# Performance work log

Hardware: AMD Instinct MI355X
Metric: run time of the kernel (lower is better)

The kernel has to match this reference:

```python
import jax, jax.numpy as jnp
import numpy as np

DIM = 512
N_GROUPS = 8
N_CODES = 1024
SUB = DIM // N_GROUPS
CB_LAMBDA = 1.0
COMMIT_LAMBDA = 0.25


def setup_inputs() -> dict:
    key = jax.random.key(0)
    k1, k2, k3 = jax.random.split(key, 3)
    x = jax.random.normal(k1, (8, DIM, 4096), dtype=jnp.float32)
    lim = 1.0 / N_CODES
    codebooks1 = jax.random.uniform(k2, (N_GROUPS, N_CODES, SUB), dtype=jnp.float32, minval=-lim, maxval=lim)
    codebooks2 = jax.random.uniform(k3, (N_GROUPS, N_CODES, SUB), dtype=jnp.float32, minval=-lim, maxval=lim)
    return {"x": x, "codebooks1": codebooks1, "codebooks2": codebooks2}


def _quantize_group(flat, cbs):
    # flat: (N, G, d), cbs: (G, K, d)
    x2 = jnp.sum(flat * flat, axis=-1, keepdims=True)          # (N, G, 1)
    e2 = jnp.sum(cbs * cbs, axis=-1)                            # (G, K)
    xe = jnp.einsum('ngd,gkd->ngk', flat, cbs)                  # (N, G, K)
    d = x2 + e2[None, :, :] - 2.0 * xe                          # (N, G, K)
    idx = jnp.argmin(d, axis=-1)                                # (N, G)
    z = cbs[jnp.arange(N_GROUPS)[None, :], idx]                 # (N, G, d)
    return z, idx


def reference(x, codebooks1, codebooks2):
    B, C, T = x.shape
    sg = jax.lax.stop_gradient
    # (B, C, T) -> (B*T, G, sub)
    xb = jnp.transpose(x, (0, 2, 1)).reshape(-1, N_GROUPS, SUB)
    residual = xb
    quantized = jnp.zeros_like(xb)
    losses = []
    all_indices = []
    for cbs in (codebooks1, codebooks2):
        z, idx = _quantize_group(residual, cbs)
        codebook_loss = jnp.mean((z - sg(residual)) ** 2)
        commit_loss = jnp.mean((sg(z) - residual) ** 2)
        losses.append(CB_LAMBDA * codebook_loss + COMMIT_LAMBDA * commit_loss)
        z_st = residual + sg(z - residual)  # straight-through
        residual = residual - z_st
        quantized = quantized + z_st
        all_indices.append(idx)
    total_loss = jnp.mean(jnp.stack(losses))
    quantized_out = jnp.transpose(quantized.reshape(B, T, C), (0, 2, 1))
    # indices in original order: layer-major, group-major -> (layers*G, B*T)
    indices = jnp.concatenate([idx.T for idx in all_indices], axis=0)
    return quantized_out, total_loss, indices
```

## Files before the change

kernel.cpp:

```cpp
#include <hip/hip_runtime.h>

#define GRP 8
#define SUBD 64
#define NCODE 1024
#define TLEN 4096
#define NBATCH 8
#define NVEC (NBATCH * TLEN)
#define QOUT (NBATCH * 512 * TLEN)
#define ROWS 128
#define NGRPS (NCODE / 8)

#define WS_E2   64
#define WS_IDX1 (WS_E2 + 65536)
#define WS_P1   (WS_IDX1 + 1048576)
#define WS_P2   (WS_P1 + 2097152)

typedef const __attribute__((address_space(1))) char GCHAR;
typedef __attribute__((address_space(3))) char LCHAR;
typedef float f2 __attribute__((ext_vector_type(2)));

__global__ __launch_bounds__(256) void k_e2(const float* __restrict__ cb1,
                                            const float* __restrict__ cb2,
                                            float* __restrict__ e2) {
    int i = blockIdx.x * 256 + threadIdx.x;
    const float* c = (i < GRP * NCODE) ? (cb1 + (size_t)i * SUBD)
                                       : (cb2 + (size_t)(i - GRP * NCODE) * SUBD);
    float s = 0.f;
#pragma unroll
    for (int d = 0; d < SUBD; ++d) s = __builtin_fmaf(c[d], c[d], s);
    e2[i] = s;
}

__global__ __launch_bounds__(256) void k_panel(const float* __restrict__ cb1,
                                               const float* __restrict__ cb2,
                                               float* __restrict__ cbP1,
                                               float* __restrict__ cbP2) {
    int i = blockIdx.x * 256 + threadIdx.x;
    int sel = i >> 13, rest = i & 8191, g = rest >> 10, k = rest & 1023;
    int grp = k >> 3, j = k & 7;
    const float* src = (sel ? cb2 : cb1) + ((size_t)g * NCODE + k) * SUBD;
    float* dst = (sel ? cbP2 : cbP1) + ((size_t)(g * NGRPS + grp) * SUBD) * 8 + j;
#pragma unroll
    for (int s = 0; s < 16; ++s) {
        float4 v = ((const float4*)src)[s];
#pragma unroll
        for (int dd = 0; dd < 4; ++dd) dst[(4 * s + dd) * 8] = ((const float*)&v)[dd];
    }
}

template <int STAGE2>
__global__ __launch_bounds__(256, 4) void k_vq(
    const float* __restrict__ x,
    const float* __restrict__ cb1,
    const float* __restrict__ cb2,
    const float* __restrict__ cbP,
    const float* __restrict__ e2,
    const int* __restrict__ idxPrev,
    int* __restrict__ idxOut,
    float* __restrict__ outIdxF,
    float* __restrict__ qout,
    double* __restrict__ lossAcc)
{
    __shared__ __align__(16) float xs[SUBD * ROWS];
    __shared__ float bdH[4 * ROWS];
    __shared__ int   biH[4 * ROWS];
    __shared__ int   i2s[ROWS];
    __shared__ double wsr[8];

    const int tid = threadIdx.x, w = tid >> 6, lane = tid & 63;
    const int g = blockIdx.y;
    const int row0 = blockIdx.x * ROWS;
    const int bz = row0 / TLEN, t0 = row0 % TLEN;
    const float* xsrc = x + ((size_t)(bz * 512 + g * SUBD)) * TLEN + t0;

    {
#pragma unroll
        for (int q = 0; q < 8; ++q) {
            int inst = w * 8 + q;
            int d = inst * 2 + (lane >> 5);
            const float* gp = xsrc + (size_t)d * TLEN + (lane & 31) * 4;
            float* lp = xs + inst * 256;
            __builtin_amdgcn_global_load_lds((GCHAR*)gp, (LCHAR*)lp, 16, 0, 0);
        }
    }
    __syncthreads();

    const int rowB = tid & 127, hi = tid >> 7;
    double ls1 = 0.0;
    int i1 = 0;
    if (STAGE2) {
        i1 = idxPrev[g * NVEC + row0 + rowB];
        const float4* z1v = (const float4*)(cb1 + ((size_t)g * NCODE + i1) * SUBD) + hi * 8;
#pragma unroll
        for (int s = 0; s < 8; ++s) {
            float4 z = z1v[s];
#pragma unroll
            for (int dd = 0; dd < 4; ++dd) {
                int d = hi * 32 + s * 4 + dd;
                float r = xs[d * ROWS + rowB];
                float zz = (&z.x)[dd];
                float tt = zz - r;
                float zst = r + tt;
                ls1 += (double)(tt * tt);
                float r2 = r - zst;
                xs[d * ROWS + rowB] = r2;
            }
        }
        __syncthreads();
    }

    const int w_u = __builtin_amdgcn_readfirstlane(w);
    const f2* xs2 = (const f2*)xs;

    f2 x2p = {0.f, 0.f};
#pragma unroll 8
    for (int d = 0; d < SUBD; ++d) {
        f2 rv = xs2[d * 64 + lane];
        x2p = __builtin_elementwise_fma(rv, rv, x2p);
    }
    const float x2a = x2p[0], x2b = x2p[1];

    const float* e2g = e2 + g * NCODE;
    float best[2] = {1e30f, 1e30f};
    int bidx[2] = {0, 0};

    for (int ib = 0; ib < 16; ++ib) {
        const float* cp = cbP + ((size_t)(g * NGRPS) + w_u * 32 + ib * 2) * (SUBD * 8);
        f2 acc[2][2][4];
#pragma unroll
        for (int r = 0; r < 2; ++r)
#pragma unroll
            for (int gg = 0; gg < 2; ++gg)
#pragma unroll
                for (int p = 0; p < 4; ++p) acc[r][gg][p] = (f2){0.f, 0.f};

#pragma unroll 4
        for (int d = 0; d < SUBD; ++d) {
            f2 rv = xs2[d * 64 + lane];
            f2 xa2 = {rv[0], rv[0]}, xb2 = {rv[1], rv[1]};
#pragma unroll
            for (int gg = 0; gg < 2; ++gg) {
                const f2* c2 = (const f2*)(cp + gg * (SUBD * 8) + d * 8);
#pragma unroll
                for (int p = 0; p < 4; ++p) {
                    f2 cv = c2[p];
                    acc[0][gg][p] = __builtin_elementwise_fma(xa2, cv, acc[0][gg][p]);
                    acc[1][gg][p] = __builtin_elementwise_fma(xb2, cv, acc[1][gg][p]);
                }
            }
        }

#pragma unroll
        for (int gg = 0; gg < 2; ++gg) {
#pragma unroll
            for (int p = 0; p < 4; ++p) {
#pragma unroll
                for (int h = 0; h < 2; ++h) {
                    int k = w_u * 256 + ib * 16 + gg * 8 + 2 * p + h;
                    float ev = e2g[k];
                    float tva = x2a + ev;
                    float da = __builtin_fmaf(-2.0f, acc[0][gg][p][h], tva);
                    if (da < best[0]) { best[0] = da; bidx[0] = k; }
                    float tvb = x2b + ev;
                    float db = __builtin_fmaf(-2.0f, acc[1][gg][p][h], tvb);
                    if (db < best[1]) { best[1] = db; bidx[1] = k; }
                }
            }
        }
    }
    bdH[w * ROWS + 2 * lane]     = best[0];
    biH[w * ROWS + 2 * lane]     = bidx[0];
    bdH[w * ROWS + 2 * lane + 1] = best[1];
    biH[w * ROWS + 2 * lane + 1] = bidx[1];
    __syncthreads();

    if (tid < ROWS) {
        float bd = bdH[tid];
        int   bi = biH[tid];
#pragma unroll
        for (int wv = 1; wv < 4; ++wv) {
            float od = bdH[wv * ROWS + tid];
            int   oi = biH[wv * ROWS + tid];
            if (od < bd) { bd = od; bi = oi; }
        }
        int nv = row0 + tid;
        outIdxF[(size_t)g * NVEC + nv] = (float)bi;
        if (!STAGE2) idxOut[g * NVEC + nv] = bi;
        else i2s[tid] = bi;
    }

    double ls2 = 0.0;
    if (STAGE2) {
        __syncthreads();
        int bi = i2s[rowB];
        const float4* z1v = (const float4*)(cb1 + ((size_t)g * NCODE + i1) * SUBD) + hi * 8;
        const float4* z2v = (const float4*)(cb2 + ((size_t)g * NCODE + bi) * SUBD) + hi * 8;
        const float* xp = xsrc + rowB;
        float* op = qout + ((size_t)(bz * 512 + g * SUBD)) * TLEN + t0 + rowB;
#pragma unroll
        for (int s = 0; s < 8; ++s) {
            float4 z1 = z1v[s];
            float4 z2 = z2v[s];
#pragma unroll
            for (int dd = 0; dd < 4; ++dd) {
                int d = hi * 32 + s * 4 + dd;
                float xv = xp[(size_t)d * TLEN];
                float r2 = xs[d * ROWS + rowB];
                float z1f = (&z1.x)[dd];
                float z2f = (&z2.x)[dd];
                float t1 = z1f - xv;
                float zst1 = xv + t1;
                float t2 = z2f - r2;
                float zst2 = r2 + t2;
                float qv = zst1 + zst2;
                op[(size_t)d * TLEN] = qv;
                ls2 += (double)(t2 * t2);
            }
        }

#pragma unroll
        for (int off = 32; off; off >>= 1) {
            ls1 += __shfl_down(ls1, off, 64);
            ls2 += __shfl_down(ls2, off, 64);
        }
        if (lane == 0) { wsr[w] = ls1; wsr[4 + w] = ls2; }
        __syncthreads();
        if (tid == 0)
            atomicAdd(lossAcc + 0, wsr[0] + wsr[1] + wsr[2] + wsr[3]);
        else if (tid == 64)
            atomicAdd(lossAcc + 1, wsr[4] + wsr[5] + wsr[6] + wsr[7]);
    }
}

__global__ void k_final(float* __restrict__ lossOut, const double* __restrict__ lossAcc) {
    double m = (lossAcc[0] + lossAcc[1]) / (double)QOUT;
    lossOut[0] = (float)(0.625 * m);
}

extern "C" void kernel_launch(void* const* d_in, const int* in_sizes, int n_in,
                              void* d_out, int out_size, void* d_ws, size_t ws_size,
                              hipStream_t stream) {
    const float* x   = (const float*)d_in[0];
    const float* cb1 = (const float*)d_in[1];
    const float* cb2 = (const float*)d_in[2];
    float* out = (float*)d_out;

    char* ws = (char*)d_ws;
    double* lossAcc = (double*)ws;
    float* e2   = (float*)(ws + WS_E2);
    int*   idx1 = (int*)(ws + WS_IDX1);
    float* cbP1 = (float*)(ws + WS_P1);
    float* cbP2 = (float*)(ws + WS_P2);

    hipMemsetAsync(ws, 0, 16, stream);

    k_e2<<<dim3(64), dim3(256), 0, stream>>>(cb1, cb2, e2);
    k_panel<<<dim3(64), dim3(256), 0, stream>>>(cb1, cb2, cbP1, cbP2);

    dim3 grid(NVEC / ROWS, GRP);
    float* outIdx = out + QOUT + 1;
    k_vq<0><<<grid, dim3(256), 0, stream>>>(x, cb1, cb2, cbP1, e2,
                                            nullptr, idx1, outIdx, nullptr, nullptr);
    k_vq<1><<<grid, dim3(256), 0, stream>>>(x, cb1, cb2, cbP2, e2 + GRP * NCODE,
                                            idx1, nullptr, outIdx + (size_t)GRP * NVEC,
                                            out, lossAcc);
    k_final<<<1, 1, 0, stream>>>(out + QOUT, lossAcc);
}
```

Baseline: 835.7 us.

## Double rows per block and compute a 4-row by 16-code register tile per lane

Each block now handles 256 rows instead of 128. Each lane computes distances for 4 rows against 16 codes, up from 2 rows, and reads x with float4 LDS loads and codebook panels with float4 global loads. Squared norms of x are precomputed into shared memory, and e2 values are loaded as float4. The goal is to halve codebook panel traffic per row and raise FMA-to-load intensity. The cost is more registers, a bigger LDS footprint and lower occupancy, with launch bounds reduced from 4 blocks to 2.

Result: slower. 962.1 us (+15.1%).

```diff
diff --git a/kernel.cpp b/kernel.cpp
--- a/kernel.cpp
+++ b/kernel.cpp
@@ -7,7 +7,7 @@
 #define NBATCH 8
 #define NVEC (NBATCH * TLEN)
 #define QOUT (NBATCH * 512 * TLEN)
-#define ROWS 128
+#define ROWS 256
 #define NGRPS (NCODE / 8)
 
 #define WS_E2   64
@@ -49,7 +49,7 @@
 }
 
 template <int STAGE2>
-__global__ __launch_bounds__(256, 4) void k_vq(
+__global__ __launch_bounds__(256, 2) void k_vq(
     const float* __restrict__ x,
     const float* __restrict__ cb1,
     const float* __restrict__ cb2,
@@ -62,6 +62,7 @@
     double* __restrict__ lossAcc)
 {
     __shared__ __align__(16) float xs[SUBD * ROWS];
+    __shared__ __align__(16) float x2s[ROWS];
     __shared__ float bdH[4 * ROWS];
     __shared__ int   biH[4 * ROWS];
     __shared__ int   i2s[ROWS];
@@ -75,112 +76,123 @@
 
     {
 #pragma unroll
-        for (int q = 0; q < 8; ++q) {
-            int inst = w * 8 + q;
-            int d = inst * 2 + (lane >> 5);
-            const float* gp = xsrc + (size_t)d * TLEN + (lane & 31) * 4;
-            float* lp = xs + inst * 256;
+        for (int q = 0; q < 16; ++q) {
+            int d = w * 16 + q;
+            const float* gp = xsrc + (size_t)d * TLEN + lane * 4;
+            float* lp = xs + d * 256;
             __builtin_amdgcn_global_load_lds((GCHAR*)gp, (LCHAR*)lp, 16, 0, 0);
         }
     }
     __syncthreads();
 
-    const int rowB = tid & 127, hi = tid >> 7;
     double ls1 = 0.0;
     int i1 = 0;
     if (STAGE2) {
-        i1 = idxPrev[g * NVEC + row0 + rowB];
-        const float4* z1v = (const float4*)(cb1 + ((size_t)g * NCODE + i1) * SUBD) + hi * 8;
-#pragma unroll
-        for (int s = 0; s < 8; ++s) {
+        i1 = idxPrev[g * NVEC + row0 + tid];
+        const float4* z1v = (const float4*)(cb1 + ((size_t)g * NCODE + i1) * SUBD);
+#pragma unroll
+        for (int s = 0; s < 16; ++s) {
             float4 z = z1v[s];
 #pragma unroll
             for (int dd = 0; dd < 4; ++dd) {
-                int d = hi * 32 + s * 4 + dd;
-                float r = xs[d * ROWS + rowB];
+                int d = 4 * s + dd;
+                float r = xs[d * ROWS + tid];
                 float zz = (&z.x)[dd];
                 float tt = zz - r;
                 float zst = r + tt;
                 ls1 += (double)(tt * tt);
                 float r2 = r - zst;
-                xs[d * ROWS + rowB] = r2;
+                xs[d * ROWS + tid] = r2;
             }
         }
         __syncthreads();
     }
 
+    {
+        float xx = 0.f;
+#pragma unroll 8
+        for (int d = 0; d < SUBD; ++d) {
+            float r = xs[d * ROWS + tid];
+            xx = __builtin_fmaf(r, r, xx);
+        }
+        x2s[tid] = xx;
+    }
+    __syncthreads();
+
     const int w_u = __builtin_amdgcn_readfirstlane(w);
-    const f2* xs2 = (const f2*)xs;
-
-    f2 x2p = {0.f, 0.f};
-#pragma unroll 8
-    for (int d = 0; d < SUBD; ++d) {
-        f2 rv = xs2[d * 64 + lane];
-        x2p = __builtin_elementwise_fma(rv, rv, x2p);
-    }
-    const float x2a = x2p[0], x2b = x2p[1];
+
+    float4 x2q = *(const float4*)(x2s + 4 * lane);
+    float x2r[4];
+#pragma unroll
+    for (int r = 0; r < 4; ++r) x2r[r] = (&x2q.x)[r];
 
     const float* e2g = e2 + g * NCODE;
-    float best[2] = {1e30f, 1e30f};
-    int bidx[2] = {0, 0};
-
-    for (int ib = 0; ib < 16; ++ib) {
-        const float* cp = cbP + ((size_t)(g * NGRPS) + w_u * 32 + ib * 2) * (SUBD * 8);
-        f2 acc[2][2][4];
-#pragma unroll
-        for (int r = 0; r < 2; ++r)
-#pragma unroll
-            for (int gg = 0; gg < 2; ++gg)
-#pragma unroll
-                for (int p = 0; p < 4; ++p) acc[r][gg][p] = (f2){0.f, 0.f};
-
-#pragma unroll 4
+    float best[4] = {1e30f, 1e30f, 1e30f, 1e30f};
+    int bidx[4] = {0, 0, 0, 0};
+
+    for (int c = 0; c < 16; ++c) {
+        const float* cp = cbP + ((size_t)(g * NGRPS) + w_u * 32 + c * 2) * (SUBD * 8);
+        const float4* cpa = (const float4*)cp;
+        const float4* cpb = (const float4*)(cp + SUBD * 8);
+        f2 acc[4][8];
+#pragma unroll
+        for (int r = 0; r < 4; ++r)
+#pragma unroll
+            for (int p = 0; p < 8; ++p) acc[r][p] = (f2){0.f, 0.f};
+
+#pragma unroll 2
         for (int d = 0; d < SUBD; ++d) {
-            f2 rv = xs2[d * 64 + lane];
-            f2 xa2 = {rv[0], rv[0]}, xb2 = {rv[1], rv[1]};
-#pragma unroll
-            for (int gg = 0; gg < 2; ++gg) {
-                const f2* c2 = (const f2*)(cp + gg * (SUBD * 8) + d * 8);
-#pragma unroll
-                for (int p = 0; p < 4; ++p) {
-                    f2 cv = c2[p];
-                    acc[0][gg][p] = __builtin_elementwise_fma(xa2, cv, acc[0][gg][p]);
-                    acc[1][gg][p] = __builtin_elementwise_fma(xb2, cv, acc[1][gg][p]);
+            float4 xq = *(const float4*)(xs + d * ROWS + 4 * lane);
+            float4 q0 = cpa[2 * d];
+            float4 q1 = cpa[2 * d + 1];
+            float4 q2 = cpb[2 * d];
+            float4 q3 = cpb[2 * d + 1];
+            f2 cv[8] = {{q0.x, q0.y}, {q0.z, q0.w}, {q1.x, q1.y}, {q1.z, q1.w},
+                        {q2.x, q2.y}, {q2.z, q2.w}, {q3.x, q3.y}, {q3.z, q3.w}};
+#pragma unroll
+            for (int r = 0; r < 4; ++r) {
+                float xv = (&xq.x)[r];
+                f2 xv2 = {xv, xv};
+#pragma unroll
+                for (int p = 0; p < 8; ++p)
+                    acc[r][p] = __builtin_elementwise_fma(xv2, cv[p], acc[r][p]);
+            }
+        }
+
+        const float4* e4 = (const float4*)(e2g + w_u * 256 + c * 16);
+        float4 e0 = e4[0], e1 = e4[1], e2q = e4[2], e3 = e4[3];
+#pragma unroll
+        for (int p = 0; p < 8; ++p) {
+#pragma unroll
+            for (int h = 0; h < 2; ++h) {
+                int j = 2 * p + h;
+                int k = w_u * 256 + c * 16 + j;
+                float ev = (j < 4) ? (&e0.x)[j]
+                         : (j < 8) ? (&e1.x)[j - 4]
+                         : (j < 12) ? (&e2q.x)[j - 8] : (&e3.x)[j - 12];
+#pragma unroll
+                for (int r = 0; r < 4; ++r) {
+                    float tv = x2r[r] + ev;
+                    float dd = __builtin_fmaf(-2.0f, acc[r][p][h], tv);
+                    if (dd < best[r]) { best[r] = dd; bidx[r] = k; }
                 }
             }
         }
-
-#pragma unroll
-        for (int gg = 0; gg < 2; ++gg) {
-#pragma unroll
-            for (int p = 0; p < 4; ++p) {
-#pragma unroll
-                for (int h = 0; h < 2; ++h) {
-                    int k = w_u * 256 + ib * 16 + gg * 8 + 2 * p + h;
-                    float ev = e2g[k];
-                    float tva = x2a + ev;
-                    float da = __builtin_fmaf(-2.0f, acc[0][gg][p][h], tva);
-                    if (da < best[0]) { best[0] = da; bidx[0] = k; }
-                    float tvb = x2b + ev;
-                    float db = __builtin_fmaf(-2.0f, acc[1][gg][p][h], tvb);
-                    if (db < best[1]) { best[1] = db; bidx[1] = k; }
-                }
-            }
-        }
-    }
-    bdH[w * ROWS + 2 * lane]     = best[0];
-    biH[w * ROWS + 2 * lane]     = bidx[0];
-    bdH[w * ROWS + 2 * lane + 1] = best[1];
-    biH[w * ROWS + 2 * lane + 1] = bidx[1];
+    }
+#pragma unroll
+    for (int r = 0; r < 4; ++r) {
+        bdH[w * ROWS + 4 * lane + r] = best[r];
+        biH[w * ROWS + 4 * lane + r] = bidx[r];
+    }
     __syncthreads();
 
-    if (tid < ROWS) {
+    {
         float bd = bdH[tid];
         int   bi = biH[tid];
 #pragma unroll
-        for (int wv = 1; wv < 4; ++wv) {
-            float od = bdH[wv * ROWS + tid];
-            int   oi = biH[wv * ROWS + tid];
+        for (int qv = 1; qv < 4; ++qv) {
+            float od = bdH[qv * ROWS + tid];
+            int   oi = biH[qv * ROWS + tid];
             if (od < bd) { bd = od; bi = oi; }
         }
         int nv = row0 + tid;
@@ -192,28 +204,28 @@
     double ls2 = 0.0;
     if (STAGE2) {
         __syncthreads();
-        int bi = i2s[rowB];
-        const float4* z1v = (const float4*)(cb1 + ((size_t)g * NCODE + i1) * SUBD) + hi * 8;
-        const float4* z2v = (const float4*)(cb2 + ((size_t)g * NCODE + bi) * SUBD) + hi * 8;
-        const float* xp = xsrc + rowB;
-        float* op = qout + ((size_t)(bz * 512 + g * SUBD)) * TLEN + t0 + rowB;
-#pragma unroll
-        for (int s = 0; s < 8; ++s) {
+        int bi = i2s[tid];
+        const float4* z1v = (const float4*)(cb1 + ((size_t)g * NCODE + i1) * SUBD);
+        const float4* z2v = (const float4*)(cb2 + ((size_t)g * NCODE + bi) * SUBD);
+        const float* xp = xsrc + tid;
+        float* op = qout + ((size_t)(bz * 512 + g * SUBD)) * TLEN + t0 + tid;
+#pragma unroll
+        for (int s = 0; s < 16; ++s) {
             float4 z1 = z1v[s];
             float4 z2 = z2v[s];
 #pragma unroll
             for (int dd = 0; dd < 4; ++dd) {
-                int d = hi * 32 + s * 4 + dd;
+                int d = 4 * s + dd;
                 float xv = xp[(size_t)d * TLEN];
-                float r2 = xs[d * ROWS + rowB];
+                float r2 = xs[d * ROWS + tid];
                 float z1f = (&z1.x)[dd];
                 float z2f = (&z2.x)[dd];
                 float t1 = z1f - xv;
                 float zst1 = xv + t1;
                 float t2 = z2f - r2;
                 float zst2 = r2 + t2;
-                float qv = zst1 + zst2;
-                op[(size_t)d * TLEN] = qv;
+                float qv2 = zst1 + zst2;
+                op[(size_t)d * TLEN] = qv2;
                 ls2 += (double)(t2 * t2);
             }
         }
```
